# Performance work log

Measured on AMD Instinct MI355X. Metric: run time of the kernel, lower is better.

Reference implementation:

```python
import jax, jax.numpy as jnp
import numpy as np

N_EMBD = 1024
HEAD_SIZE = 64
TOP_K = 32


def setup_inputs() -> dict:
    key = jax.random.key(0)
    ks = jax.random.split(key, 10)
    B, T, C, D, N = 4, 2048, N_EMBD, HEAD_SIZE, 16384
    s = 1.0 / np.sqrt(C)
    return {
        "x": jax.random.normal(ks[0], (B, T, C), jnp.float32),
        "mem_keys": jax.random.normal(ks[1], (B, N, D), jnp.float32),
        "mem_vals": jax.random.normal(ks[2], (B, N, D), jnp.float32),
        "Wq": jax.random.normal(ks[3], (C, D), jnp.float32) * s,
        "bq": jnp.zeros((D,), jnp.float32),
        "Wk": jax.random.normal(ks[4], (C, D), jnp.float32) * s,
        "bk": jnp.zeros((D,), jnp.float32),
        "Wv": jax.random.normal(ks[5], (C, D), jnp.float32) * s,
        "bv": jnp.zeros((D,), jnp.float32),
        "gate": jax.random.normal(ks[6], (1,), jnp.float32),
    }


def reference(x, mem_keys, mem_vals, Wq, bq, Wk, bk, Wv, bv, gate):
    B, T, C = x.shape
    scale = 1.0 / jnp.sqrt(jnp.asarray(C, x.dtype))  # note: scaled by n_embd, as in source
    q = x @ Wq + bq  # [B,T,D]
    k = x @ Wk + bk
    v = x @ Wv + bv
    # causal self-attention
    att = jnp.einsum("btd,bsd->bts", q, k) * scale
    causal = jnp.tril(jnp.ones((T, T), bool))
    att = jnp.where(causal[None], att, -jnp.inf)
    att = jax.nn.softmax(att, axis=-1)
    out = jnp.einsum("bts,bsd->btd", att, v)  # [B,T,D]
    # kNN memory attention: top-k inner-product search over memory bank
    scores = jnp.einsum("btd,bnd->btn", q, mem_keys)  # [B,T,N]
    _, idx = jax.lax.top_k(scores, TOP_K)  # [B,T,K]
    mem_k = jnp.take_along_axis(mem_keys[:, None], idx[..., None], axis=2)  # [B,T,K,D]
    mem_v = jnp.take_along_axis(mem_vals[:, None], idx[..., None], axis=2)  # [B,T,K,D]
    mem_att = jax.nn.softmax(jnp.einsum("btd,btkd->btk", q, mem_k) * scale, axis=-1)
    mem_out = jnp.einsum("btk,btkd->btd", mem_att, mem_v)  # [B,T,D]
    g = gate[0]
    md_out = out * g + mem_out * (1.0 - g)  # gated combine; dropout is identity at eval
    return md_out
```

## Files before the change

### kernel.cpp

```cpp
#include <hip/hip_runtime.h>
#include <math.h>

#define B_ 4
#define T_ 2048
#define C_ 1024
#define D_ 64
#define N_ 16384
#define K_ 32
#define SCALE 0.03125f
#define NEGINF -3.402823e38f

typedef __attribute__((ext_vector_type(8))) short short8_t;
typedef __attribute__((ext_vector_type(4))) float f32x4;

__device__ __forceinline__ unsigned short f2bf(float x) {
    union { float f; unsigned u; } a; a.f = x;
    const unsigned r = a.u + 0x7fffu + ((a.u >> 16) & 1u);
    return (unsigned short)(r >> 16);
}
__device__ __forceinline__ float bf2f(unsigned short h) {
    union { unsigned u; float f; } a; a.u = ((unsigned)h) << 16;
    return a.f;
}

__global__ __launch_bounds__(256) void wfrag_prep_kernel(
    const float* __restrict__ Wq, const float* __restrict__ Wk,
    const float* __restrict__ Wv,
    unsigned short* __restrict__ whfrag, unsigned short* __restrict__ wlfrag)
{
    const int tid = threadIdx.x;
    const int w = tid >> 6, lane = tid & 63;
    const int id = blockIdx.x * 4 + w;
    const int ct = id >> 5, ks = id & 31;
    const float* W = (ct < 4) ? Wq : (ct < 8) ? Wk : Wv;
    const int colw = (ct & 3) * 16 + (lane & 15);
    const int k0 = ks * 32 + (lane >> 4) * 8;
    unsigned short* dh = whfrag + (size_t)id * 512 + (size_t)lane * 8;
    unsigned short* dl = wlfrag + (size_t)id * 512 + (size_t)lane * 8;
    #pragma unroll
    for (int j = 0; j < 8; ++j) {
        const float val = W[(size_t)(k0 + j) * D_ + colw];
        const unsigned short h = f2bf(val);
        dh[j] = h;
        dl[j] = f2bf(val - bf2f(h));
    }
}

__global__ __launch_bounds__(256) void qkv_mfma_kernel(
    const float* __restrict__ x,
    const unsigned short* __restrict__ whfrag, const unsigned short* __restrict__ wlfrag,
    const float* __restrict__ bq, const float* __restrict__ bk,
    const float* __restrict__ bv,
    float* __restrict__ q, float* __restrict__ k, float* __restrict__ v)
{
    __shared__ unsigned short xh[32][136], xl[32][136];
    const int tid = threadIdx.x;
    const int w = tid >> 6, lane = tid & 63;
    const int row0 = blockIdx.x * 32;
    const int rt = w & 1;
    const int ct0 = (w >> 1) * 6;

    f32x4 acc[6];
    #pragma unroll
    for (int i = 0; i < 6; ++i) {
        const int ct = ct0 + i;
        const float* bias = (ct < 4) ? bq : (ct < 8) ? bk : bv;
        const float bb = bias[(ct & 3) * 16 + (lane & 15)];
        acc[i] = (f32x4){bb, bb, bb, bb};
    }

    for (int kc = 0; kc < 8; ++kc) {
        __syncthreads();
        #pragma unroll
        for (int p = 0; p < 4; ++p) {
            const int fi = tid + p * 256;
            const int row = fi >> 5, c4 = fi & 31;
            const float4 xv =
                *(const float4*)(x + (size_t)(row0 + row) * C_ + kc * 128 + c4 * 4);
            const unsigned short h0 = f2bf(xv.x), h1 = f2bf(xv.y);
            const unsigned short h2 = f2bf(xv.z), h3 = f2bf(xv.w);
            xh[row][c4 * 4 + 0] = h0;  xl[row][c4 * 4 + 0] = f2bf(xv.x - bf2f(h0));
            xh[row][c4 * 4 + 1] = h1;  xl[row][c4 * 4 + 1] = f2bf(xv.y - bf2f(h1));
            xh[row][c4 * 4 + 2] = h2;  xl[row][c4 * 4 + 2] = f2bf(xv.z - bf2f(h2));
            xh[row][c4 * 4 + 3] = h3;  xl[row][c4 * 4 + 3] = f2bf(xv.w - bf2f(h3));
        }
        __syncthreads();
        #pragma unroll
        for (int ks = 0; ks < 4; ++ks) {
            const int aoff = ks * 32 + (lane >> 4) * 8;
            const short8_t ah = *(const short8_t*)&xh[rt * 16 + (lane & 15)][aoff];
            const short8_t al = *(const short8_t*)&xl[rt * 16 + (lane & 15)][aoff];
            #pragma unroll
            for (int i = 0; i < 6; ++i) {
                const size_t tb = ((size_t)(ct0 + i) * 32 + kc * 4 + ks) * 512
                                + (size_t)lane * 8;
                const short8_t wh = *(const short8_t*)(whfrag + tb);
                const short8_t wl = *(const short8_t*)(wlfrag + tb);
                acc[i] = __builtin_amdgcn_mfma_f32_16x16x32_bf16(ah, wh, acc[i], 0, 0, 0);
                acc[i] = __builtin_amdgcn_mfma_f32_16x16x32_bf16(ah, wl, acc[i], 0, 0, 0);
                acc[i] = __builtin_amdgcn_mfma_f32_16x16x32_bf16(al, wh, acc[i], 0, 0, 0);
            }
        }
    }

    #pragma unroll
    for (int i = 0; i < 6; ++i) {
        const int ct = ct0 + i;
        float* o = (ct < 4) ? q : (ct < 8) ? k : v;
        const int col = (ct & 3) * 16 + (lane & 15);
        const int rbase = row0 + rt * 16 + (lane >> 4) * 4;
        #pragma unroll
        for (int r = 0; r < 4; ++r)
            o[(size_t)(rbase + r) * D_ + col] = acc[i][r];
    }
}

__global__ __launch_bounds__(256) void kfrag_prep_kernel(
    const float* __restrict__ keys, unsigned short* __restrict__ khi,
    unsigned short* __restrict__ klo)
{
    const int tid = threadIdx.x;
    const int lane = tid & 63;
    const int ks = (tid >> 6) & 1;
    const int b  = blockIdx.x >> 9;
    const int nt = ((blockIdx.x & 511) << 1) | (tid >> 7);
    const int key = nt * 16 + (lane & 15);
    const float* src = keys + ((size_t)b * N_ + key) * D_ + ks * 32 + (lane >> 4) * 8;
    const size_t o = (((size_t)b * 1024 + nt) * 2 + ks) * 512 + (size_t)lane * 8;
    #pragma unroll
    for (int j = 0; j < 8; ++j) {
        const float xv = src[j];
        const unsigned short h = f2bf(xv);
        khi[o + j] = h;
        klo[o + j] = f2bf(xv - bf2f(h));
    }
}

__global__ __launch_bounds__(256) void causal_prep_kernel(
    const float* __restrict__ k, const float* __restrict__ v,
    unsigned short* __restrict__ kcfrag, unsigned short* __restrict__ vfrag)
{
    __shared__ float vtile[64][68];
    const int tid = threadIdx.x;
    const int b = blockIdx.x >> 5;
    const int n64 = blockIdx.x & 31;
    const int w = tid >> 6, lane = tid & 63;
    const int q16 = lane & 15, g = lane >> 4;

    const float4* in4 = (const float4*)(v + ((size_t)b * T_ + n64 * 64) * D_);
    #pragma unroll
    for (int p = 0; p < 4; ++p) {
        const int fi = tid + p * 256;
        const int row = fi >> 4, c4 = fi & 15;
        *(float4*)&vtile[row][c4 * 4] = in4[fi];
    }

    {
        const int key = (n64 * 4 + w) * 16 + q16;
        #pragma unroll
        for (int ks = 0; ks < 2; ++ks) {
            const float* src = k + ((size_t)b * T_ + key) * D_ + ks * 32 + g * 8;
            const float4 x0 = *(const float4*)(src);
            const float4 x1 = *(const float4*)(src + 4);
            unsigned short* dst = kcfrag
                + ((((size_t)b * 128 + n64 * 4 + w) * 2 + ks) * 512) + (size_t)lane * 8;
            dst[0] = f2bf(x0.x); dst[1] = f2bf(x0.y); dst[2] = f2bf(x0.z); dst[3] = f2bf(x0.w);
            dst[4] = f2bf(x1.x); dst[5] = f2bf(x1.y); dst[6] = f2bf(x1.z); dst[7] = f2bf(x1.w);
        }
    }
    __syncthreads();

    #pragma unroll
    for (int ks = 0; ks < 2; ++ks) {
        unsigned short* dst = vfrag
            + ((((size_t)b * 32 + n64) * 8 + ks * 4 + w) * 512) + (size_t)lane * 8;
        #pragma unroll
        for (int j = 0; j < 8; ++j)
            dst[j] = f2bf(vtile[ks * 32 + g * 8 + j][w * 16 + q16]);
    }
}

__global__ __launch_bounds__(256) void causal_flash_kernel(
    const float* __restrict__ qg,
    const unsigned short* __restrict__ kcfrag, const unsigned short* __restrict__ vfrag,
    float* __restrict__ outc)
{
    __shared__ unsigned int plds[64][36];
    __shared__ float po[4][64][17];
    __shared__ float pml[4][2][16];
    const int tid = threadIdx.x;
    const int w = tid >> 6, lane = tid & 63;
    const int q16 = lane & 15, g = lane >> 4;
    const int b = blockIdx.x >> 7;
    const int qt = blockIdx.x & 127;
    const int t0 = qt * 16;
    const int qglob = t0 + q16;
    const int n64 = (qt >> 2) + 1;

    short8_t qf[2];
    #pragma unroll
    for (int ks = 0; ks < 2; ++ks) {
        const float* src = qg + ((size_t)b * T_ + qglob) * D_ + ks * 32 + g * 8;
        const float4 x0 = *(const float4*)(src);
        const float4 x1 = *(const float4*)(src + 4);
        qf[ks][0] = (short)f2bf(x0.x); qf[ks][1] = (short)f2bf(x0.y);
        qf[ks][2] = (short)f2bf(x0.z); qf[ks][3] = (short)f2bf(x0.w);
        qf[ks][4] = (short)f2bf(x1.x); qf[ks][5] = (short)f2bf(x1.y);
        qf[ks][6] = (short)f2bf(x1.z); qf[ks][7] = (short)f2bf(x1.w);
    }

    float m = -1.0e30f, l = 0.f;
    f32x4 o[4];
    #pragma unroll
    for (int dt = 0; dt < 4; ++dt) o[dt] = (f32x4){0.f, 0.f, 0.f, 0.f};

    const int qrow = w * 16 + q16;

    for (int n = w; n < n64; n += 4) {
        short8_t kf[4][2];
        #pragma unroll
        for (int a = 0; a < 4; ++a)
            #pragma unroll
            for (int ks = 0; ks < 2; ++ks)
                kf[a][ks] = *(const short8_t*)(kcfrag
                    + ((((size_t)b * 128 + n * 4 + a) * 2 + ks) * 512) + (size_t)lane * 8);
        f32x4 st[4];
        #pragma unroll
        for (int a = 0; a < 4; ++a) {
            st[a] = (f32x4){0.f, 0.f, 0.f, 0.f};
            st[a] = __builtin_amdgcn_mfma_f32_16x16x32_bf16(kf[a][0], qf[0], st[a], 0, 0, 0);
            st[a] = __builtin_amdgcn_mfma_f32_16x16x32_bf16(kf[a][1], qf[1], st[a], 0, 0, 0);
        }

        float sv[4][4];
        float pm = -1.0e30f;
        #pragma unroll
        for (int a = 0; a < 4; ++a)
            #pragma unroll
            for (int r = 0; r < 4; ++r) {
                const int kk = n * 64 + a * 16 + g * 4 + r;
                float x = st[a][r] * SCALE;
                x = (kk <= qglob) ? x : -1.0e31f;
                sv[a][r] = x;
                pm = fmaxf(pm, x);
            }
        pm = fmaxf(pm, __shfl_xor(pm, 16));
        pm = fmaxf(pm, __shfl_xor(pm, 32));
        const float mn = fmaxf(m, pm);
        const float al = __expf(m - mn);
        float rs = 0.f;
        float ev[4][4];
        #pragma unroll
        for (int a = 0; a < 4; ++a)
            #pragma unroll
            for (int r = 0; r < 4; ++r) {
                const float e = __expf(sv[a][r] - mn);
                ev[a][r] = e;
                rs += e;
            }
        rs += __shfl_xor(rs, 16);
        rs += __shfl_xor(rs, 32);
        l = l * al + rs;
        m = mn;
        #pragma unroll
        for (int dt = 0; dt < 4; ++dt) o[dt] *= al;

        #pragma unroll
        for (int a = 0; a < 4; ++a)
            #pragma unroll
            for (int rp = 0; rp < 2; ++rp)
                plds[qrow][a * 8 + g * 2 + rp] =
                    (unsigned)f2bf(ev[a][2 * rp]) | ((unsigned)f2bf(ev[a][2 * rp + 1]) << 16);
        #pragma unroll
        for (int ks = 0; ks < 2; ++ks) {
            const short8_t pf = *(const short8_t*)&plds[qrow][ks * 16 + g * 4];
            #pragma unroll
            for (int dt = 0; dt < 4; ++dt) {
                const short8_t vf = *(const short8_t*)(vfrag
                    + ((((size_t)b * 32 + n) * 8 + ks * 4 + dt) * 512) + (size_t)lane * 8);
                o[dt] = __builtin_amdgcn_mfma_f32_16x16x32_bf16(vf, pf, o[dt], 0, 0, 0);
            }
        }
    }

    #pragma unroll
    for (int dt = 0; dt < 4; ++dt)
        #pragma unroll
        for (int r = 0; r < 4; ++r)
            po[w][dt * 16 + g * 4 + r][q16] = o[dt][r];
    if (g == 0) { pml[w][0][q16] = m; pml[w][1][q16] = l; }
    __syncthreads();

    {
        const int q = tid & 15;
        const int dgrp = tid >> 4;
        float mw[4], lw[4];
        #pragma unroll
        for (int ww = 0; ww < 4; ++ww) { mw[ww] = pml[ww][0][q]; lw[ww] = pml[ww][1][q]; }
        const float M = fmaxf(fmaxf(mw[0], mw[1]), fmaxf(mw[2], mw[3]));
        float wgt[4], L = 0.f;
        #pragma unroll
        for (int ww = 0; ww < 4; ++ww) {
            wgt[ww] = __expf(mw[ww] - M);
            L += lw[ww] * wgt[ww];
        }
        const float inv = 1.0f / L;
        float4 res;
        float* rp = &res.x;
        #pragma unroll
        for (int i = 0; i < 4; ++i) {
            const int d = dgrp * 4 + i;
            float s = 0.f;
            #pragma unroll
            for (int ww = 0; ww < 4; ++ww) s += po[ww][d][q] * wgt[ww];
            rp[i] = s * inv;
        }
        *(float4*)(outc + ((size_t)b * T_ + t0 + q) * D_ + dgrp * 4) = res;
    }
}

__global__ __launch_bounds__(512) void knn_mfma_kernel(
    const float* __restrict__ qg,
    const unsigned short* __restrict__ khi, const unsigned short* __restrict__ klo,
    const float* __restrict__ mem_vals, const float* __restrict__ outc,
    const float* __restrict__ gate, float* __restrict__ outp)
{
    __shared__ float sc_lds[2][16][260];
    const int tid = threadIdx.x;
    const int w = tid >> 6, lane = tid & 63;
    const int bid = blockIdx.x;
    const int b  = (bid & 7) >> 1;
    const int qt = ((bid >> 3) << 1) | (bid & 1);
    const int t0 = qt * 16;

    short8_t qh[2], ql[2];
    {
        const int qrow = t0 + (lane & 15);
        const float* qs = qg + ((size_t)b * T_ + qrow) * D_ + (lane >> 4) * 8;
        #pragma unroll
        for (int ks2 = 0; ks2 < 2; ++ks2) {
            #pragma unroll
            for (int j = 0; j < 8; ++j) {
                const float xv = qs[ks2 * 32 + j];
                const unsigned short h = f2bf(xv);
                qh[ks2][j] = (short)h;
                ql[ks2][j] = (short)f2bf(xv - bf2f(h));
            }
        }
    }

    const int qrow4 = (lane >> 4) * 4;
    const int c16 = lane & 15;

#define LOADFRAGS(CC, KH, KL)                                                  \
    {                                                                          \
        _Pragma("unroll")                                                      \
        for (int tt = 0; tt < 2; ++tt) {                                       \
            const int tl = w + 8 * tt;                                         \
            const size_t kb = (((size_t)b * 1024 + (size_t)(CC) * 16 + tl) * 2) * 512 \
                            + (size_t)lane * 8;                                \
            KH[tt][0] = *(const short8_t*)(khi + kb);                          \
            KH[tt][1] = *(const short8_t*)(khi + kb + 512);                    \
            KL[tt][0] = *(const short8_t*)(klo + kb);                          \
            KL[tt][1] = *(const short8_t*)(klo + kb + 512);                    \
        }                                                                      \
    }

#define MFMAWRITE(BUF, KH, KL)                                                 \
    {                                                                          \
        _Pragma("unroll")                                                      \
        for (int tt = 0; tt < 2; ++tt) {                                       \
            const int tl = w + 8 * tt;                                         \
            f32x4 acc = {0.f, 0.f, 0.f, 0.f};                                  \
            acc = __builtin_amdgcn_mfma_f32_16x16x32_bf16(qh[0], KH[tt][0], acc, 0, 0, 0); \
            acc = __builtin_amdgcn_mfma_f32_16x16x32_bf16(qh[1], KH[tt][1], acc, 0, 0, 0); \
            acc = __builtin_amdgcn_mfma_f32_16x16x32_bf16(qh[0], KL[tt][0], acc, 0, 0, 0); \
            acc = __builtin_amdgcn_mfma_f32_16x16x32_bf16(qh[1], KL[tt][1], acc, 0, 0, 0); \
            acc = __builtin_amdgcn_mfma_f32_16x16x32_bf16(ql[0], KH[tt][0], acc, 0, 0, 0); \
            acc = __builtin_amdgcn_mfma_f32_16x16x32_bf16(ql[1], KH[tt][1], acc, 0, 0, 0); \
            const int col = tl * 16 + c16;                                     \
            _Pragma("unroll")                                                  \
            for (int r = 0; r < 4; ++r) sc_lds[BUF][qrow4 + r][col] = acc[r];  \
        }                                                                      \
    }

    float rv[2];  int rid_[2];  float t32[2];
    #pragma unroll
    for (int qq = 0; qq < 2; ++qq) {
        rv[qq] = NEGINF; rid_[qq] = 0x7fffffff; t32[qq] = NEGINF;
    }

    {
        short8_t kh[2][2], kl[2][2];
        LOADFRAGS(0, kh, kl);
        MFMAWRITE(0, kh, kl);
    }
    __syncthreads();

    for (int c = 0; c < 64; ++c) {
        short8_t kh[2][2], kl[2][2];
        if (c < 63) LOADFRAGS(c + 1, kh, kl);

        float s4[2][4];
        #pragma unroll
        for (int qq = 0; qq < 2; ++qq)
            *(float4*)(&s4[qq][0]) = *(const float4*)&sc_lds[c & 1][w * 2 + qq][lane * 4];

        if (c == 0) {
            #pragma unroll
            for (int qq = 0; qq < 2; ++qq) {
                float lmax = NEGINF; int lslot = 0;
                #pragma unroll
                for (int j = 0; j < 4; ++j)
                    if (s4[qq][j] > lmax) { lmax = s4[qq][j]; lslot = j; }
                for (int it = 0; it < 32; ++it) {
                    float wm = lmax;
                    #pragma unroll
                    for (int off = 32; off; off >>= 1)
                        wm = fmaxf(wm, __shfl_xor(wm, off));
                    const unsigned long long bal = __ballot(lmax == wm);
                    const int winner = __ffsll((unsigned long long)bal) - 1;
                    const int wslot  = __shfl(lslot, winner);
                    const int widx   = (winner << 2) + (wslot & 3);
                    const unsigned long long gb = __ballot((lane < K_) && (rv[qq] > wm));
                    const int pos = __popcll(gb);
                    const float sv = __shfl_up(rv[qq], 1);
                    const int   si = __shfl_up(rid_[qq], 1);
                    if (lane > pos)       { rv[qq] = sv; rid_[qq] = si; }
                    else if (lane == pos) { rv[qq] = wm; rid_[qq] = widx; }
                    if (lane == winner) {
                        float nm = NEGINF; int ns = 0;
                        #pragma unroll
                        for (int j = 0; j < 4; ++j) {
                            const float vj = (j == lslot) ? NEGINF : s4[qq][j];
                            s4[qq][j] = vj;
                            if (vj > nm) { nm = vj; ns = j; }
                        }
                        lmax = nm; lslot = ns;
                    }
                }
                t32[qq] = __shfl(rv[qq], 31);
            }
        } else {
            #pragma unroll
            for (int qq = 0; qq < 2; ++qq) {
                #pragma unroll
                for (int j = 0; j < 4; ++j) {
                    unsigned long long bb = __ballot(s4[qq][j] > t32[qq]);
                    while (bb) {
                        const int L = __ffsll(bb) - 1;
                        bb &= bb - 1;
                        const float xv = __shfl(s4[qq][j], L);
                        const int xi = (c << 8) + (L << 2) + j;
                        const unsigned long long gb =
                            __ballot((lane < K_) && (rv[qq] > xv));
                        const int pos = __popcll(gb);
                        const float sv = __shfl_up(rv[qq], 1);
                        const int   si = __shfl_up(rid_[qq], 1);
                        if (lane > pos)       { rv[qq] = sv; rid_[qq] = si; }
                        else if (lane == pos) { rv[qq] = xv; rid_[qq] = xi; }
                    }
                }
                t32[qq] = __shfl(rv[qq], 31);
            }
        }

        if (c < 63) MFMAWRITE((c + 1) & 1, kh, kl);
        __syncthreads();
    }

#undef LOADFRAGS
#undef MFMAWRITE

    const float gv = gate[0];
    const float* vb = mem_vals + (size_t)b * N_ * D_;
    #pragma unroll
    for (int qq = 0; qq < 2; ++qq) {
        const float m = __shfl(rv[qq], 0);
        float wgt = (lane < K_) ? __expf((rv[qq] - m) * SCALE) : 0.f;
        float ssum = wgt;
        #pragma unroll
        for (int off = 32; off; off >>= 1) ssum += __shfl_xor(ssum, off);
        float acc = 0.f;
        for (int i = 0; i < K_; ++i) {
            const float wi = __shfl(wgt, i);
            const int   ii = __shfl(rid_[qq], i);
            acc += wi * vb[(size_t)ii * D_ + lane];
        }
        const size_t o = ((size_t)(b * T_ + t0 + w * 2 + qq)) * D_ + lane;
        outp[o] = outc[o] * gv + (acc / ssum) * (1.f - gv);
    }
}

extern "C" void kernel_launch(void* const* d_in, const int* in_sizes, int n_in,
                              void* d_out, int out_size, void* d_ws, size_t ws_size,
                              hipStream_t stream) {
    const float* x        = (const float*)d_in[0];
    const float* mem_keys = (const float*)d_in[1];
    const float* mem_vals = (const float*)d_in[2];
    const float* Wq       = (const float*)d_in[3];
    const float* bq       = (const float*)d_in[4];
    const float* Wk       = (const float*)d_in[5];
    const float* bk       = (const float*)d_in[6];
    const float* Wv       = (const float*)d_in[7];
    const float* bv       = (const float*)d_in[8];
    const float* gate     = (const float*)d_in[9];
    float* out = (float*)d_out;

    const size_t btd = (size_t)B_ * T_ * D_;
    float* q    = (float*)d_ws;
    float* k    = q + btd;
    float* v    = k + btd;
    float* outc = v + btd;
    unsigned short* khi    = (unsigned short*)(outc + btd);
    unsigned short* klo    = khi + (size_t)B_ * N_ * D_;
    unsigned short* kcfrag = klo + (size_t)B_ * N_ * D_;
    unsigned short* vfrag  = kcfrag + btd;
    unsigned short* whfrag = vfrag + btd;
    unsigned short* wlfrag = whfrag + (size_t)384 * 512;

    wfrag_prep_kernel<<<96, 256, 0, stream>>>(Wq, Wk, Wv, whfrag, wlfrag);
    qkv_mfma_kernel<<<B_ * T_ / 32, 256, 0, stream>>>(x, whfrag, wlfrag,
                                                      bq, bk, bv, q, k, v);
    kfrag_prep_kernel<<<B_ * 512, 256, 0, stream>>>(mem_keys, khi, klo);
    causal_prep_kernel<<<B_ * 32, 256, 0, stream>>>(k, v, kcfrag, vfrag);
    causal_flash_kernel<<<B_ * 128, 256, 0, stream>>>(q, kcfrag, vfrag, outc);
    knn_mfma_kernel<<<512, 512, 0, stream>>>(q, khi, klo, mem_vals, outc, gate, out);
}
```

Before: 272.4 us.

## Double kNN chunk size, merge candidate ballots per lane, reverse causal block order

The kNN kernel now handles 512 memory keys per iteration instead of 256, which halves the loop trip count and the number of __syncthreads barriers, at the cost of more registers and twice the LDS for the score buffer. Top-k candidate detection now takes one ballot per lane over the max of its four scores, using a per-lane mask, instead of four separate ballots. The causal flash kernel schedules query tiles in reverse so the longest causal rows launch first, which should improve load balance. The larger fragment arrays may raise register pressure and reduce occupancy.

```diff
diff --git a/kernel.cpp b/kernel.cpp
--- a/kernel.cpp
+++ b/kernel.cpp
@@ -192,7 +192,7 @@
     const int w = tid >> 6, lane = tid & 63;
     const int q16 = lane & 15, g = lane >> 4;
     const int b = blockIdx.x >> 7;
-    const int qt = blockIdx.x & 127;
+    const int qt = 127 - (blockIdx.x & 127);
     const int t0 = qt * 16;
     const int qglob = t0 + q16;
     const int n64 = (qt >> 2) + 1;
@@ -325,7 +325,7 @@
     const float* __restrict__ mem_vals, const float* __restrict__ outc,
     const float* __restrict__ gate, float* __restrict__ outp)
 {
-    __shared__ float sc_lds[2][16][260];
+    __shared__ float sc_lds[2][16][512];
     const int tid = threadIdx.x;
     const int w = tid >> 6, lane = tid & 63;
     const int bid = blockIdx.x;
@@ -355,9 +355,9 @@
 #define LOADFRAGS(CC, KH, KL)                                                  \
     {                                                                          \
         _Pragma("unroll")                                                      \
-        for (int tt = 0; tt < 2; ++tt) {                                       \
+        for (int tt = 0; tt < 4; ++tt) {                                       \
             const int tl = w + 8 * tt;                                         \
-            const size_t kb = (((size_t)b * 1024 + (size_t)(CC) * 16 + tl) * 2) * 512 \
+            const size_t kb = (((size_t)b * 1024 + (size_t)(CC) * 32 + tl) * 2) * 512 \
                             + (size_t)lane * 8;                                \
             KH[tt][0] = *(const short8_t*)(khi + kb);                          \
             KH[tt][1] = *(const short8_t*)(khi + kb + 512);                    \
@@ -369,7 +369,7 @@
 #define MFMAWRITE(BUF, KH, KL)                                                 \
     {                                                                          \
         _Pragma("unroll")                                                      \
-        for (int tt = 0; tt < 2; ++tt) {                                       \
+        for (int tt = 0; tt < 4; ++tt) {                                       \
             const int tl = w + 8 * tt;                                         \
             f32x4 acc = {0.f, 0.f, 0.f, 0.f};                                  \
             acc = __builtin_amdgcn_mfma_f32_16x16x32_bf16(qh[0], KH[tt][0], acc, 0, 0, 0); \
@@ -384,6 +384,34 @@
         }                                                                      \
     }
 
+#define STREAM4(S4, CC, HALF, QQ)                                              \
+    {                                                                          \
+        const float m01 = fmaxf(S4[0], S4[1]);                                 \
+        const float m23 = fmaxf(S4[2], S4[3]);                                 \
+        unsigned mask4 = (S4[0] > t32[QQ] ? 1u : 0u) | (S4[1] > t32[QQ] ? 2u : 0u) \
+                       | (S4[2] > t32[QQ] ? 4u : 0u) | (S4[3] > t32[QQ] ? 8u : 0u); \
+        unsigned long long bb = __ballot(fmaxf(m01, m23) > t32[QQ]);           \
+        while (bb) {                                                           \
+            const int L = __ffsll(bb) - 1;                                     \
+            bb &= bb - 1;                                                      \
+            const unsigned mL = (unsigned)__shfl((int)mask4, L);               \
+            _Pragma("unroll")                                                  \
+            for (int j = 0; j < 4; ++j) {                                      \
+                if ((mL >> j) & 1u) {                                          \
+                    const float xv = __shfl(S4[j], L);                         \
+                    const int xi = ((CC) << 9) + ((HALF) << 8) + (L << 2) + j; \
+                    const unsigned long long gb =                              \
+                        __ballot((lane < K_) && (rv[QQ] > xv));                \
+                    const int pos = __popcll(gb);                              \
+                    const float sv = __shfl_up(rv[QQ], 1);                     \
+                    const int   si = __shfl_up(rid_[QQ], 1);                   \
+                    if (lane > pos)       { rv[QQ] = sv; rid_[QQ] = si; }      \
+                    else if (lane == pos) { rv[QQ] = xv; rid_[QQ] = xi; }      \
+                }                                                              \
+            }                                                                  \
+        }                                                                      \
+    }
+
     float rv[2];  int rid_[2];  float t32[2];
     #pragma unroll
     for (int qq = 0; qq < 2; ++qq) {
@@ -391,28 +419,25 @@
     }
 
     {
-        short8_t kh[2][2], kl[2][2];
+        short8_t kh[4][2], kl[4][2];
         LOADFRAGS(0, kh, kl);
         MFMAWRITE(0, kh, kl);
     }
     __syncthreads();
 
-    for (int c = 0; c < 64; ++c) {
-        short8_t kh[2][2], kl[2][2];
-        if (c < 63) LOADFRAGS(c + 1, kh, kl);
-
-        float s4[2][4];
-        #pragma unroll
-        for (int qq = 0; qq < 2; ++qq)
-            *(float4*)(&s4[qq][0]) = *(const float4*)&sc_lds[c & 1][w * 2 + qq][lane * 4];
+    for (int c = 0; c < 32; ++c) {
+        short8_t kh[4][2], kl[4][2];
+        if (c < 31) LOADFRAGS(c + 1, kh, kl);
 
         if (c == 0) {
             #pragma unroll
             for (int qq = 0; qq < 2; ++qq) {
+                float s4[4];
+                *(float4*)s4 = *(const float4*)&sc_lds[0][w * 2 + qq][lane * 4];
                 float lmax = NEGINF; int lslot = 0;
                 #pragma unroll
                 for (int j = 0; j < 4; ++j)
-                    if (s4[qq][j] > lmax) { lmax = s4[qq][j]; lslot = j; }
+                    if (s4[j] > lmax) { lmax = s4[j]; lslot = j; }
                 for (int it = 0; it < 32; ++it) {
                     float wm = lmax;
                     #pragma unroll
@@ -432,45 +457,38 @@
                         float nm = NEGINF; int ns = 0;
                         #pragma unroll
                         for (int j = 0; j < 4; ++j) {
-                            const float vj = (j == lslot) ? NEGINF : s4[qq][j];
-                            s4[qq][j] = vj;
+                            const float vj = (j == lslot) ? NEGINF : s4[j];
+                            s4[j] = vj;
                             if (vj > nm) { nm = vj; ns = j; }
                         }
                         lmax = nm; lslot = ns;
                     }
                 }
                 t32[qq] = __shfl(rv[qq], 31);
+                float s4b[4];
+                *(float4*)s4b = *(const float4*)&sc_lds[0][w * 2 + qq][256 + lane * 4];
+                STREAM4(s4b, 0, 1, qq)
+                t32[qq] = __shfl(rv[qq], 31);
             }
         } else {
             #pragma unroll
             for (int qq = 0; qq < 2; ++qq) {
-                #pragma unroll
-                for (int j = 0; j < 4; ++j) {
-                    unsigned long long bb = __ballot(s4[qq][j] > t32[qq]);
-                    while (bb) {
-                        const int L = __ffsll(bb) - 1;
-                        bb &= bb - 1;
-                        const float xv = __shfl(s4[qq][j], L);
-                        const int xi = (c << 8) + (L << 2) + j;
-                        const unsigned long long gb =
-                            __ballot((lane < K_) && (rv[qq] > xv));
-                        const int pos = __popcll(gb);
-                        const float sv = __shfl_up(rv[qq], 1);
-                        const int   si = __shfl_up(rid_[qq], 1);
-                        if (lane > pos)       { rv[qq] = sv; rid_[qq] = si; }
-                        else if (lane == pos) { rv[qq] = xv; rid_[qq] = xi; }
-                    }
-                }
+                float s4a[4], s4b[4];
+                *(float4*)s4a = *(const float4*)&sc_lds[c & 1][w * 2 + qq][lane * 4];
+                *(float4*)s4b = *(const float4*)&sc_lds[c & 1][w * 2 + qq][256 + lane * 4];
+                STREAM4(s4a, c, 0, qq)
+                STREAM4(s4b, c, 1, qq)
                 t32[qq] = __shfl(rv[qq], 31);
             }
         }
 
-        if (c < 63) MFMAWRITE((c + 1) & 1, kh, kl);
+        if (c < 31) MFMAWRITE((c + 1) & 1, kh, kl);
         __syncthreads();
     }
 
 #undef LOADFRAGS
 #undef MFMAWRITE
+#undef STREAM4
 
     const float gv = gate[0];
     const float* vb = mem_vals + (size_t)b * N_ * D_;
```

Result: slower. 315.8 us (+15.9%).
